# Kernel optimization log

Measured on AMD Instinct MI355X. Metric: run time of the kernel, lower is better.

## Reference

```python
import jax, jax.numpy as jnp
import numpy as np

N_NODES = 50000
N_EDGES = 1600000
NFEAT = 512
HIDDEN = 128
NUM_CLASSES = 40
DROPOUT = 0.5


def setup_inputs() -> dict:
    key = jax.random.key(0)
    ks = jax.random.split(key, 8)
    x = jax.random.normal(ks[0], (N_NODES, NFEAT), dtype=jnp.float32)
    edge_row = jax.random.randint(ks[1], (N_EDGES,), 0, N_NODES, dtype=jnp.int32)
    edge_col = jax.random.randint(ks[2], (N_EDGES,), 0, N_NODES, dtype=jnp.int32)
    edge_vals = jax.random.uniform(ks[3], (N_EDGES,), dtype=jnp.float32)
    # uniform(-stdv, stdv) init as in reset_parameters
    stdv1 = 1.0 / np.sqrt(HIDDEN)
    stdv2 = 1.0 / np.sqrt(NUM_CLASSES)
    W1 = jax.random.uniform(ks[4], (NFEAT, HIDDEN), dtype=jnp.float32, minval=-stdv1, maxval=stdv1)
    b1 = jax.random.uniform(ks[5], (HIDDEN,), dtype=jnp.float32, minval=-stdv1, maxval=stdv1)
    W2 = jax.random.uniform(ks[6], (HIDDEN, NUM_CLASSES), dtype=jnp.float32, minval=-stdv2, maxval=stdv2)
    b2 = jax.random.uniform(ks[7], (NUM_CLASSES,), dtype=jnp.float32, minval=-stdv2, maxval=stdv2)
    return {"x": x, "edge_row": edge_row, "edge_col": edge_col, "edge_vals": edge_vals,
            "W1": W1, "b1": b1, "W2": W2, "b2": b2}


def _spmm(edge_row, edge_col, edge_vals, support):
    # out[i] = sum_{e: row[e]==i} vals[e] * support[col[e]]  (sparse adj @ support)
    msgs = support[edge_col] * edge_vals[:, None]  # [E, F]
    return jax.ops.segment_sum(msgs, edge_row, num_segments=N_NODES)


def _dropout(x, rate, key):
    keep = 1.0 - rate
    mask = jax.random.bernoulli(key, keep, x.shape)
    return jnp.where(mask, x / keep, jnp.zeros((), x.dtype))


def reference(x, edge_row, edge_col, edge_vals, W1, b1, W2, b2):
    # layer 1: GCN conv + bias + relu + dropout (training=True)
    h = _spmm(edge_row, edge_col, edge_vals, x @ W1) + b1  # [N, H]
    h = jax.nn.relu(h)
    h = _dropout(h, DROPOUT, jax.random.key(42))
    # layer 2: GCN conv + bias + relu
    out = _spmm(edge_row, edge_col, edge_vals, h @ W2) + b2  # [N, C]
    return jax.nn.relu(out)
```

## Files before the change

kernel.cpp:

```cpp
#include <hip/hip_runtime.h>
#include <hip/hip_bf16.h>

#define N_NODES 50000
#define N_EDGES 1600000
#define NFEAT   512
#define HIDDEN  128
#define NCLASS  40

#define NBUCK 391
#define ROWS_PER_BUCKET 128
#define BUCK_PAD 4608

#define W1T_BLOCKS 256
#define GEMM1_BLOCKS 391
#define PART_T 2048
#define PART_BLOCKS 782

#define FUSED_LDS 21560

typedef short short8 __attribute__((ext_vector_type(8)));
typedef float f32x4  __attribute__((ext_vector_type(4)));

__device__ __forceinline__ unsigned short f2bu(float f) {
  __hip_bfloat16 h = __float2bfloat16(f);
  return *reinterpret_cast<unsigned short*>(&h);
}

__device__ __forceinline__ unsigned rotl32(unsigned x, int n) {
  return (x << n) | (x >> (32 - n));
}

__device__ __forceinline__ unsigned threefry_bits(unsigned x1) {
  unsigned x0 = 0u;
  const unsigned ks0 = 0u, ks1 = 42u, ks2 = 0x1BD11BDAu ^ 42u;
  x0 += ks0; x1 += ks1;
#define TFR(r) { x0 += x1; x1 = rotl32(x1, (r)); x1 ^= x0; }
  TFR(13) TFR(15) TFR(26) TFR(6)
  x0 += ks1; x1 += ks2 + 1u;
  TFR(17) TFR(29) TFR(16) TFR(24)
  x0 += ks2; x1 += ks0 + 2u;
  TFR(13) TFR(15) TFR(26) TFR(6)
  x0 += ks0; x1 += ks1 + 3u;
  TFR(17) TFR(29) TFR(16) TFR(24)
  x0 += ks1; x1 += ks2 + 4u;
  TFR(13) TFR(15) TFR(26) TFR(6)
  x0 += ks2; x1 += ks0 + 5u;
#undef TFR
  return x0 ^ x1;
}

__global__ __launch_bounds__(256) void init_w1t_kernel(
    const float* __restrict__ W1, unsigned short* __restrict__ W1T,
    int* __restrict__ gcur) {
  if (blockIdx.x < W1T_BLOCKS) {
    int id = blockIdx.x * 256 + threadIdx.x;
    int n = id & 127, k = id >> 7;
    W1T[n * NFEAT + k] = f2bu(W1[k * HIDDEN + n]);
  } else {
    int b = threadIdx.x;
    if (b < NBUCK) gcur[b] = b * BUCK_PAD;
    b += 256;
    if (b < NBUCK) gcur[b] = b * BUCK_PAD;
  }
}

__device__ __forceinline__ void gemm1_body(
    int bid, char* smem, const float* __restrict__ x,
    const unsigned short* __restrict__ W1T,
    unsigned short* __restrict__ support) {
  short8* As = (short8*)smem;
  short8* Bs = (short8*)(smem + 8192);
  const int t = threadIdx.x;
  const int lane = t & 63;
  const int w = t >> 6;
  const int quad = lane >> 4;
  const int l15 = lane & 15;
  const int node_base = bid * 128;
  const int mbase = (w >> 1) * 64;
  const int nbase = (w & 1) * 64;

  f32x4 acc[4][4] = {};

  for (int k0 = 0; k0 < NFEAT; k0 += 32) {
#pragma unroll
    for (int i = 0; i < 2; i++) {
      int lin = i * 256 + t;
      int n = lin >> 2, q = lin & 3;
      int row = node_base + n;
      if (row >= N_NODES) row = N_NODES - 1;
      const float* src = &x[(size_t)row * NFEAT + k0 + q * 8];
      float4 a = *(const float4*)src;
      float4 b = *(const float4*)(src + 4);
      short8 p;
      p[0] = (short)f2bu(a.x); p[1] = (short)f2bu(a.y);
      p[2] = (short)f2bu(a.z); p[3] = (short)f2bu(a.w);
      p[4] = (short)f2bu(b.x); p[5] = (short)f2bu(b.y);
      p[6] = (short)f2bu(b.z); p[7] = (short)f2bu(b.w);
      As[q * 128 + n] = p;
      Bs[q * 128 + n] = *(const short8*)&W1T[(size_t)n * NFEAT + k0 + q * 8];
    }
    __syncthreads();
    short8 af[4], bfr[4];
#pragma unroll
    for (int mt = 0; mt < 4; mt++)
      af[mt] = As[quad * 128 + mbase + mt * 16 + l15];
#pragma unroll
    for (int nt = 0; nt < 4; nt++)
      bfr[nt] = Bs[quad * 128 + nbase + nt * 16 + l15];
#pragma unroll
    for (int mt = 0; mt < 4; mt++)
#pragma unroll
      for (int nt = 0; nt < 4; nt++)
        acc[mt][nt] = __builtin_amdgcn_mfma_f32_16x16x32_bf16(
            af[mt], bfr[nt], acc[mt][nt], 0, 0, 0);
    __syncthreads();
  }

#pragma unroll
  for (int mt = 0; mt < 4; mt++)
#pragma unroll
    for (int nt = 0; nt < 4; nt++)
#pragma unroll
      for (int r = 0; r < 4; r++) {
        int row = node_base + mbase + mt * 16 + quad * 4 + r;
        int col = nbase + nt * 16 + l15;
        if (row < N_NODES)
          support[(size_t)row * HIDDEN + col] = f2bu(acc[mt][nt][r]);
      }
}

__device__ __forceinline__ void partition_body(
    int bid, char* smem, const int* __restrict__ erow,
    const int* __restrict__ ecol, const float* __restrict__ evals,
    int* __restrict__ gcur, uint2* __restrict__ eb) {
  uint2* sorted = (uint2*)smem;
  int* cnt   = (int*)(smem + 16384);
  int* shift = (int*)(smem + 16384 + 1564);
  int* ssc   = (int*)(smem + 16384 + 3128);
  const int t = threadIdx.x;
  const int base = bid * PART_T;

  if (t < NBUCK) cnt[t] = 0;
  if (t + 256 < NBUCK) cnt[t + 256] = 0;
  __syncthreads();

  uint2 er[8];
  unsigned short loc[8];
#pragma unroll
  for (int k = 0; k < 8; k++) {
    int idx = base + k * 256 + t;
    if (idx < N_EDGES) {
      int r = erow[idx];
      er[k].y = (unsigned)r;
      er[k].x = (unsigned)ecol[idx] | ((unsigned)f2bu(evals[idx]) << 16);
      loc[k] = (unsigned short)atomicAdd(&cnt[r >> 7], 1);
    } else {
      er[k].y = 0xffffffffu;
    }
  }
  __syncthreads();

  ssc[t] = (t < NBUCK) ? cnt[t] : 0;
  ssc[t + 256] = (t + 256 < NBUCK) ? cnt[t + 256] : 0;
  __syncthreads();
#pragma unroll
  for (int off = 1; off < 512; off <<= 1) {
    int v0 = (t >= off) ? ssc[t - off] : 0;
    int v1 = ssc[t + 256 - off];
    __syncthreads();
    ssc[t] += v0; ssc[t + 256] += v1;
    __syncthreads();
  }

  for (int b = t; b < NBUCK; b += 256) {
    int c = cnt[b];
    if (c > 0) {
      int lb = ssc[b] - c;
      int gb = atomicAdd(&gcur[b], c);
      shift[b] = gb - lb;
    }
  }
#pragma unroll
  for (int k = 0; k < 8; k++) {
    if (er[k].y != 0xffffffffu) {
      int b = (int)(er[k].y >> 7);
      sorted[ssc[b] - cnt[b] + (int)loc[k]] = er[k];
    }
  }
  __syncthreads();

  const int total = ssc[NBUCK - 1];
  for (int i = t; i < total; i += 256) {
    uint2 e = sorted[i];
    eb[shift[e.y >> 7] + i] = e;
  }
}

__global__ __launch_bounds__(256) void part_gemm1_kernel(
    const int* __restrict__ erow, const int* __restrict__ ecol,
    const float* __restrict__ evals, int* __restrict__ gcur,
    uint2* __restrict__ eb, const float* __restrict__ x,
    const unsigned short* __restrict__ W1T,
    unsigned short* __restrict__ support) {
  __shared__ char smem[FUSED_LDS];
  if (blockIdx.x < PART_BLOCKS)
    partition_body(blockIdx.x, smem, erow, ecol, evals, gcur, eb);
  else
    gemm1_body(blockIdx.x - PART_BLOCKS, smem, x, W1T, support);
}

__global__ __launch_bounds__(512) void csr_build_kernel(
    const uint2* __restrict__ eb, const int* __restrict__ gcur,
    unsigned* __restrict__ csr, int* __restrict__ rowptr,
    int* __restrict__ rowend) {
  __shared__ int cnt[ROWS_PER_BUCKET];
  __shared__ int sc[ROWS_PER_BUCKET];
  __shared__ int cur[ROWS_PER_BUCKET];
  const int t = threadIdx.x;
  const int b = blockIdx.x;
  if (t < ROWS_PER_BUCKET) cnt[t] = 0;
  __syncthreads();
  const int beg = b * BUCK_PAD;
  const int end = gcur[b];
  for (int j = beg + t; j < end; j += 512)
    atomicAdd(&cnt[eb[j].y & 127u], 1);
  __syncthreads();
  if (t < ROWS_PER_BUCKET) sc[t] = cnt[t];
  __syncthreads();
#pragma unroll
  for (int off = 1; off < ROWS_PER_BUCKET; off <<= 1) {
    int v = 0;
    if (t >= off && t < ROWS_PER_BUCKET) v = sc[t - off];
    __syncthreads();
    if (t < ROWS_PER_BUCKET) sc[t] += v;
    __syncthreads();
  }
  if (t < ROWS_PER_BUCKET) {
    int excl = sc[t] - cnt[t];
    cur[t] = excl;
    int row = b * ROWS_PER_BUCKET + t;
    if (row < N_NODES) {
      rowptr[row] = beg + excl;
      rowend[row] = beg + sc[t];
    }
  }
  __syncthreads();
  for (int j = beg + t; j < end; j += 512) {
    uint2 e = eb[j];
    int p = atomicAdd(&cur[e.y & 127u], 1);
    csr[beg + p] = e.x;
  }
}

__global__ __launch_bounds__(256) void spmm1_fused(
    const unsigned* __restrict__ csr, const int* __restrict__ rowptr,
    const int* __restrict__ rowend,
    const unsigned* __restrict__ sup,
    const float* __restrict__ b1, unsigned* __restrict__ h) {
  const int row = blockIdx.x * 4 + (threadIdx.x >> 6);
  const int lane = threadIdx.x & 63;
  const int beg = rowptr[row], end = rowend[row];
  float ax = 0.f, ay = 0.f;
  int j = beg;
  for (; j + 15 < end; j += 16) {
    unsigned p[16], u[16];
#pragma unroll
    for (int k = 0; k < 16; k++) p[k] = csr[j + k];
#pragma unroll
    for (int k = 0; k < 16; k++) u[k] = sup[(p[k] & 0xffffu) * 64 + lane];
#pragma unroll
    for (int k = 0; k < 16; k++) {
      float v = __uint_as_float(p[k] & 0xffff0000u);
      ax += v * __uint_as_float(u[k] << 16);
      ay += v * __uint_as_float(u[k] & 0xffff0000u);
    }
  }
  for (; j + 7 < end; j += 8) {
    unsigned p[8], u[8];
#pragma unroll
    for (int k = 0; k < 8; k++) p[k] = csr[j + k];
#pragma unroll
    for (int k = 0; k < 8; k++) u[k] = sup[(p[k] & 0xffffu) * 64 + lane];
#pragma unroll
    for (int k = 0; k < 8; k++) {
      float v = __uint_as_float(p[k] & 0xffff0000u);
      ax += v * __uint_as_float(u[k] << 16);
      ay += v * __uint_as_float(u[k] & 0xffff0000u);
    }
  }
  for (; j + 1 < end; j += 2) {
    unsigned p0 = csr[j], p1 = csr[j + 1];
    unsigned u0 = sup[(p0 & 0xffffu) * 64 + lane];
    unsigned u1 = sup[(p1 & 0xffffu) * 64 + lane];
    float v0 = __uint_as_float(p0 & 0xffff0000u);
    float v1 = __uint_as_float(p1 & 0xffff0000u);
    ax += v0 * __uint_as_float(u0 << 16) + v1 * __uint_as_float(u1 << 16);
    ay += v0 * __uint_as_float(u0 & 0xffff0000u) +
          v1 * __uint_as_float(u1 & 0xffff0000u);
  }
  if (j < end) {
    unsigned p0 = csr[j];
    unsigned u0 = sup[(p0 & 0xffffu) * 64 + lane];
    float v0 = __uint_as_float(p0 & 0xffff0000u);
    ax += v0 * __uint_as_float(u0 << 16);
    ay += v0 * __uint_as_float(u0 & 0xffff0000u);
  }
  const unsigned i0 = (unsigned)row * HIDDEN + lane * 2;
  float vx = fmaxf(ax + b1[lane * 2], 0.f);
  float vy = fmaxf(ay + b1[lane * 2 + 1], 0.f);
  vx = (threefry_bits(i0) >> 31) ? 0.f : 2.f * vx;
  vy = (threefry_bits(i0 + 1) >> 31) ? 0.f : 2.f * vy;
  h[(unsigned)row * 64 + lane] = (unsigned)f2bu(vx) | ((unsigned)f2bu(vy) << 16);
}

__global__ __launch_bounds__(256) void gemm2_kernel(
    const uint4* __restrict__ h,
    const float* __restrict__ W2, unsigned short* __restrict__ h2) {
  __shared__ float Hs[64][132];
  __shared__ float Ws[40][132];
  const int t = threadIdx.x;
  const int node_base = blockIdx.x * 64;
#pragma unroll
  for (int i = 0; i < 4; i++) {
    int lin = i * 256 + t;
    int nloc = lin >> 4, c8 = lin & 15;
    int n = node_base + nloc;
    if (n >= N_NODES) n = N_NODES - 1;
    uint4 u = h[(size_t)n * 16 + c8];
    float* d = &Hs[nloc][c8 * 8];
    d[0] = __uint_as_float(u.x << 16); d[1] = __uint_as_float(u.x & 0xffff0000u);
    d[2] = __uint_as_float(u.y << 16); d[3] = __uint_as_float(u.y & 0xffff0000u);
    d[4] = __uint_as_float(u.z << 16); d[5] = __uint_as_float(u.z & 0xffff0000u);
    d[6] = __uint_as_float(u.w << 16); d[7] = __uint_as_float(u.w & 0xffff0000u);
  }
#pragma unroll
  for (int i = 0; i < 20; i++) {
    int l = t + i * 256;
    int k = l / NCLASS, f = l % NCLASS;
    Ws[f][k] = W2[l];
  }
  __syncthreads();
  const int nloc = t >> 2;
  const int fb = t & 3;
  const int n = node_base + nloc;
  float acc[10];
#pragma unroll
  for (int j = 0; j < 10; j++) acc[j] = 0.f;
  for (int k = 0; k < HIDDEN; k += 4) {
    float4 a = *(const float4*)&Hs[nloc][k];
#pragma unroll
    for (int j = 0; j < 10; j++) {
      float4 wv = *(const float4*)&Ws[fb + 4 * j][k];
      acc[j] += a.x * wv.x + a.y * wv.y + a.z * wv.z + a.w * wv.w;
    }
  }
  if (n < N_NODES) {
#pragma unroll
    for (int j = 0; j < 10; j++)
      h2[(size_t)n * NCLASS + fb + 4 * j] = f2bu(acc[j]);
  }
}

__global__ __launch_bounds__(256) void spmm2_fused(
    const unsigned* __restrict__ csr, const int* __restrict__ rowptr,
    const int* __restrict__ rowend,
    const unsigned* __restrict__ h2u,
    const float* __restrict__ b2, float* __restrict__ out) {
  const int row = blockIdx.x * 4 + (threadIdx.x >> 6);
  const int lane = threadIdx.x & 63;
  const int half = lane >> 5;
  const int il = lane & 31;
  const unsigned ilc = (il < 20) ? (unsigned)il : 19u;
  const int beg = rowptr[row], end = rowend[row];
  float ax = 0.f, ay = 0.f;
  int j = beg + half;
  for (; j + 6 < end; j += 8) {
    unsigned p[4], u[4];
#pragma unroll
    for (int k = 0; k < 4; k++) p[k] = csr[j + 2 * k];
#pragma unroll
    for (int k = 0; k < 4; k++) u[k] = h2u[(p[k] & 0xffffu) * 20 + ilc];
#pragma unroll
    for (int k = 0; k < 4; k++) {
      float v = __uint_as_float(p[k] & 0xffff0000u);
      ax += v * __uint_as_float(u[k] << 16);
      ay += v * __uint_as_float(u[k] & 0xffff0000u);
    }
  }
  for (; j + 2 < end; j += 4) {
    unsigned p0 = csr[j];
    unsigned p1 = csr[j + 2];
    unsigned u0 = h2u[(p0 & 0xffffu) * 20 + ilc];
    unsigned u1 = h2u[(p1 & 0xffffu) * 20 + ilc];
    float v0 = __uint_as_float(p0 & 0xffff0000u);
    float v1 = __uint_as_float(p1 & 0xffff0000u);
    ax += v0 * __uint_as_float(u0 << 16) + v1 * __uint_as_float(u1 << 16);
    ay += v0 * __uint_as_float(u0 & 0xffff0000u) +
          v1 * __uint_as_float(u1 & 0xffff0000u);
  }
  for (; j < end; j += 2) {
    unsigned p0 = csr[j];
    unsigned u0 = h2u[(p0 & 0xffffu) * 20 + ilc];
    float v0 = __uint_as_float(p0 & 0xffff0000u);
    ax += v0 * __uint_as_float(u0 << 16);
    ay += v0 * __uint_as_float(u0 & 0xffff0000u);
  }
  ax += __shfl_xor(ax, 32);
  ay += __shfl_xor(ay, 32);
  if (half == 0 && il < 20) {
    float2 r;
    r.x = fmaxf(ax + b2[il * 2], 0.f);
    r.y = fmaxf(ay + b2[il * 2 + 1], 0.f);
    *(float2*)&out[(unsigned)row * NCLASS + il * 2] = r;
  }
}

extern "C" void kernel_launch(void* const* d_in, const int* in_sizes, int n_in,
                              void* d_out, int out_size, void* d_ws,
                              size_t ws_size, hipStream_t stream) {
  const float* x     = (const float*)d_in[0];
  const int*   erow  = (const int*)d_in[1];
  const int*   ecol  = (const int*)d_in[2];
  const float* evals = (const float*)d_in[3];
  const float* W1    = (const float*)d_in[4];
  const float* b1    = (const float*)d_in[5];
  const float* W2    = (const float*)d_in[6];
  const float* b2    = (const float*)d_in[7];
  float* out = (float*)d_out;

  char* base = (char*)d_ws;
  unsigned short* support = (unsigned short*)base;
  uint2*          eb  = (uint2*)(base + 12800000);
  unsigned*       h   = (unsigned*)(base + 12800000);
  unsigned short* h2  = (unsigned short*)(base + 27213824);
  unsigned short* W1T = (unsigned short*)(base + 31213824);
  unsigned*       csr = (unsigned*)(base + 31344896);
  int* rowptr = (int*)(base + 38551808);
  int* rowend = (int*)(base + 38751808);
  int* gcur   = (int*)(base + 38951808);

  init_w1t_kernel<<<W1T_BLOCKS + 1, 256, 0, stream>>>(W1, W1T, gcur);
  part_gemm1_kernel<<<PART_BLOCKS + GEMM1_BLOCKS, 256, 0, stream>>>(
      erow, ecol, evals, gcur, eb, x, W1T, support);
  csr_build_kernel<<<NBUCK, 512, 0, stream>>>(eb, gcur, csr, rowptr, rowend);
  spmm1_fused<<<N_NODES / 4, 256, 0, stream>>>(csr, rowptr, rowend,
                                               (const unsigned*)support, b1, h);
  gemm2_kernel<<<(N_NODES + 63) / 64, 256, 0, stream>>>((const uint4*)h, W2,
                                                        h2);
  spmm2_fused<<<N_NODES / 4, 256, 0, stream>>>(csr, rowptr, rowend,
                                               (const unsigned*)h2, b2, out);
}
```

Baseline: 331.1 us.

## Fuse hidden-to-class GEMM into SpMM1 epilogue and enlarge partition tiles

The second dense GEMM (h @ W2) moves into the spmm1 kernel. Each wave writes its dropout-applied hidden row to LDS, and 40 lanes compute the class outputs against a W2 copy in shared memory. The h2 result is written directly as packed bf16 pairs. This removes one kernel launch and the round trip of the bf16 hidden matrix through global memory. In exchange, every spmm1 block reloads the 20KB W2 into LDS, which may lower occupancy, and only 40 of 64 lanes do the small GEMM. Separately, edge-partition blocks now each handle 4096 edges instead of 2048, halving the partition block count, with a larger LDS sort buffer.

```diff
diff --git a/kernel.cpp b/kernel.cpp
--- a/kernel.cpp
+++ b/kernel.cpp
@@ -13,10 +13,10 @@
 
 #define W1T_BLOCKS 256
 #define GEMM1_BLOCKS 391
-#define PART_T 2048
-#define PART_BLOCKS 782
-
-#define FUSED_LDS 21560
+#define PART_T 4096
+#define PART_BLOCKS 391
+
+#define FUSED_LDS 37944
 
 typedef short short8 __attribute__((ext_vector_type(8)));
 typedef float f32x4  __attribute__((ext_vector_type(4)));
@@ -134,9 +134,9 @@
     const int* __restrict__ ecol, const float* __restrict__ evals,
     int* __restrict__ gcur, uint2* __restrict__ eb) {
   uint2* sorted = (uint2*)smem;
-  int* cnt   = (int*)(smem + 16384);
-  int* shift = (int*)(smem + 16384 + 1564);
-  int* ssc   = (int*)(smem + 16384 + 3128);
+  int* cnt   = (int*)(smem + 32768);
+  int* shift = (int*)(smem + 32768 + 1564);
+  int* ssc   = (int*)(smem + 32768 + 3128);
   const int t = threadIdx.x;
   const int base = bid * PART_T;
 
@@ -144,10 +144,10 @@
   if (t + 256 < NBUCK) cnt[t + 256] = 0;
   __syncthreads();
 
-  uint2 er[8];
-  unsigned short loc[8];
-#pragma unroll
-  for (int k = 0; k < 8; k++) {
+  uint2 er[16];
+  unsigned short loc[16];
+#pragma unroll
+  for (int k = 0; k < 16; k++) {
     int idx = base + k * 256 + t;
     if (idx < N_EDGES) {
       int r = erow[idx];
@@ -181,7 +181,7 @@
     }
   }
 #pragma unroll
-  for (int k = 0; k < 8; k++) {
+  for (int k = 0; k < 16; k++) {
     if (er[k].y != 0xffffffffu) {
       int b = (int)(er[k].y >> 7);
       sorted[ssc[b] - cnt[b] + (int)loc[k]] = er[k];
@@ -256,9 +256,18 @@
     const unsigned* __restrict__ csr, const int* __restrict__ rowptr,
     const int* __restrict__ rowend,
     const unsigned* __restrict__ sup,
-    const float* __restrict__ b1, unsigned* __restrict__ h) {
-  const int row = blockIdx.x * 4 + (threadIdx.x >> 6);
-  const int lane = threadIdx.x & 63;
+    const float* __restrict__ b1, const float* __restrict__ W2,
+    unsigned* __restrict__ h2u) {
+  __shared__ float Ws[HIDDEN * NCLASS];
+  __shared__ unsigned hrow[4][64];
+  const int t = threadIdx.x;
+#pragma unroll
+  for (int i = 0; i < 20; i++) Ws[i * 256 + t] = W2[i * 256 + t];
+  __syncthreads();
+
+  const int row = blockIdx.x * 4 + (t >> 6);
+  const int wv = t >> 6;
+  const int lane = t & 63;
   const int beg = rowptr[row], end = rowend[row];
   float ax = 0.f, ay = 0.f;
   int j = beg;
@@ -310,54 +319,23 @@
   float vy = fmaxf(ay + b1[lane * 2 + 1], 0.f);
   vx = (threefry_bits(i0) >> 31) ? 0.f : 2.f * vx;
   vy = (threefry_bits(i0 + 1) >> 31) ? 0.f : 2.f * vy;
-  h[(unsigned)row * 64 + lane] = (unsigned)f2bu(vx) | ((unsigned)f2bu(vy) << 16);
-}
-
-__global__ __launch_bounds__(256) void gemm2_kernel(
-    const uint4* __restrict__ h,
-    const float* __restrict__ W2, unsigned short* __restrict__ h2) {
-  __shared__ float Hs[64][132];
-  __shared__ float Ws[40][132];
-  const int t = threadIdx.x;
-  const int node_base = blockIdx.x * 64;
-#pragma unroll
-  for (int i = 0; i < 4; i++) {
-    int lin = i * 256 + t;
-    int nloc = lin >> 4, c8 = lin & 15;
-    int n = node_base + nloc;
-    if (n >= N_NODES) n = N_NODES - 1;
-    uint4 u = h[(size_t)n * 16 + c8];
-    float* d = &Hs[nloc][c8 * 8];
-    d[0] = __uint_as_float(u.x << 16); d[1] = __uint_as_float(u.x & 0xffff0000u);
-    d[2] = __uint_as_float(u.y << 16); d[3] = __uint_as_float(u.y & 0xffff0000u);
-    d[4] = __uint_as_float(u.z << 16); d[5] = __uint_as_float(u.z & 0xffff0000u);
-    d[6] = __uint_as_float(u.w << 16); d[7] = __uint_as_float(u.w & 0xffff0000u);
-  }
-#pragma unroll
-  for (int i = 0; i < 20; i++) {
-    int l = t + i * 256;
-    int k = l / NCLASS, f = l % NCLASS;
-    Ws[f][k] = W2[l];
-  }
-  __syncthreads();
-  const int nloc = t >> 2;
-  const int fb = t & 3;
-  const int n = node_base + nloc;
-  float acc[10];
-#pragma unroll
-  for (int j = 0; j < 10; j++) acc[j] = 0.f;
-  for (int k = 0; k < HIDDEN; k += 4) {
-    float4 a = *(const float4*)&Hs[nloc][k];
-#pragma unroll
-    for (int j = 0; j < 10; j++) {
-      float4 wv = *(const float4*)&Ws[fb + 4 * j][k];
-      acc[j] += a.x * wv.x + a.y * wv.y + a.z * wv.z + a.w * wv.w;
-    }
-  }
-  if (n < N_NODES) {
-#pragma unroll
-    for (int j = 0; j < 10; j++)
-      h2[(size_t)n * NCLASS + fb + 4 * j] = f2bu(acc[j]);
+  hrow[wv][lane] = (unsigned)f2bu(vx) | ((unsigned)f2bu(vy) << 16);
+  __syncthreads();
+
+  float accv = 0.f;
+  if (lane < NCLASS) {
+#pragma unroll 8
+    for (int i = 0; i < 64; i++) {
+      unsigned u = hrow[wv][i];
+      float h0 = __uint_as_float(u << 16);
+      float h1 = __uint_as_float(u & 0xffff0000u);
+      accv += h0 * Ws[(2 * i) * NCLASS + lane] +
+              h1 * Ws[(2 * i + 1) * NCLASS + lane];
+    }
+    float other = __shfl_xor(accv, 1);
+    if (!(lane & 1))
+      h2u[(unsigned)row * 20 + (lane >> 1)] =
+          (unsigned)f2bu(accv) | ((unsigned)f2bu(other) << 16);
   }
 }
 
@@ -431,8 +409,7 @@
   char* base = (char*)d_ws;
   unsigned short* support = (unsigned short*)base;
   uint2*          eb  = (uint2*)(base + 12800000);
-  unsigned*       h   = (unsigned*)(base + 12800000);
-  unsigned short* h2  = (unsigned short*)(base + 27213824);
+  unsigned*       h2  = (unsigned*)(base + 27213824);
   unsigned short* W1T = (unsigned short*)(base + 31213824);
   unsigned*       csr = (unsigned*)(base + 31344896);
   int* rowptr = (int*)(base + 38551808);
@@ -443,10 +420,8 @@
   part_gemm1_kernel<<<PART_BLOCKS + GEMM1_BLOCKS, 256, 0, stream>>>(
       erow, ecol, evals, gcur, eb, x, W1T, support);
   csr_build_kernel<<<NBUCK, 512, 0, stream>>>(eb, gcur, csr, rowptr, rowend);
-  spmm1_fused<<<N_NODES / 4, 256, 0, stream>>>(csr, rowptr, rowend,
-                                               (const unsigned*)support, b1, h);
-  gemm2_kernel<<<(N_NODES + 63) / 64, 256, 0, stream>>>((const uint4*)h, W2,
-                                                        h2);
+  spmm1_fused<<<N_NODES / 4, 256, 0, stream>>>(
+      csr, rowptr, rowend, (const unsigned*)support, b1, W2, h2);
   spmm2_fused<<<N_NODES / 4, 256, 0, stream>>>(csr, rowptr, rowend,
                                                (const unsigned*)h2, b2, out);
 }
```

After: 318.1 us. 3.9% less time.
